# Performance work log

Measured on AMD Instinct MI355X. Metric: run time of the kernel, lower is better.

## Reference

```python
import jax, jax.numpy as jnp
import numpy as np

N = 100000      # num_nodes
E = 6400000     # num edges
D = 128         # embedding_dim
R = 8           # num_roles
ALPHA = 0.15
ITERS = 10

def setup_inputs() -> dict:
    key = jax.random.key(0)
    k1, k2, k3, k4, k5 = jax.random.split(key, 5)
    edge_index = jax.random.randint(k1, (2, E), 0, N)
    batch_nodes = jax.random.randint(k2, (N,), 0, N)
    importance_emb = jax.random.normal(k3, (N, D), dtype=jnp.float32)
    resizer_W = jax.random.normal(k4, (D, 2), dtype=jnp.float32) * (1.0 / np.sqrt(D))
    resizer_b = jnp.zeros((2,), dtype=jnp.float32)
    # xavier_uniform for behavior_matrix [R, 4]
    limit = np.sqrt(6.0 / (R + 4))
    behavior_matrix = jax.random.uniform(k5, (R, 4), minval=-limit, maxval=limit, dtype=jnp.float32)
    return {
        'edge_index': edge_index,
        'batch_nodes': batch_nodes,
        'importance_emb': importance_emb,
        'resizer_W': resizer_W,
        'resizer_b': resizer_b,
        'behavior_matrix': behavior_matrix,
    }

def reference(edge_index, batch_nodes, importance_emb, resizer_W, resizer_b, behavior_matrix):
    src, dst = edge_index[0], edge_index[1]
    num_edges = src.shape[0]
    # out-degrees via segment_sum (== bincount)
    out_deg = jax.ops.segment_sum(jnp.ones((num_edges,), jnp.float32), src, num_segments=N)
    inv_deg_src = 1.0 / jnp.maximum(out_deg, 1.0)[src]  # [E], clamp(min=1)

    # approximate_pagerank: 10 iterations of gather -> scale -> scatter_add
    def body(pr, _):
        contrib = (1.0 - ALPHA) * pr[src] * inv_deg_src
        new_pr = jax.ops.segment_sum(contrib, dst, num_segments=N) + ALPHA / N
        return new_pr, None
    pr0 = jnp.full((N,), 1.0 / N, dtype=jnp.float32)
    pagerank, _ = jax.lax.scan(body, pr0, None, length=ITERS)

    # resizer: single Linear(D, 2)
    emb2 = importance_emb @ resizer_W + resizer_b  # [B, 2]

    # X = [deg[batch], pagerank[batch], emb2] -> [B, 4]
    X = jnp.concatenate([out_deg[batch_nodes][:, None],
                         pagerank[batch_nodes][:, None],
                         emb2], axis=1)

    # lstsq(H.T, X.T): A = H.T is [4, R], underdetermined -> minimum-norm
    # solution Z = A^T (A A^T)^{-1} X^T ; W = Z^T  -> [B, R]
    A = behavior_matrix.T                      # [4, R]
    G = A @ A.T                                # [4, 4]
    W = (A.T @ jnp.linalg.solve(G, X.T)).T     # [B, R]

    # F.normalize(W, p=2, dim=1)
    norm = jnp.linalg.norm(W, axis=1, keepdims=True)
    roles = W / jnp.maximum(norm, 1e-12)
    return roles
```

## Files before the change

### kernel.cpp

```cpp
#include <hip/hip_runtime.h>
#include <math.h>

#define N_NODES 100000
#define N_EDGES 6400000
#define DIM     128
#define NROLES  8
#define ALPHA   0.15f
#define PR_ITERS 10

#define DSH      8
#define DBS      256
#define NDB      391
#define SSH      9
#define SBS      512
#define NSB      196
#define NBT      587
#define NBLK_BIN 512
#define CHUNK    12500
#define SEG      4
#define SBIN     1568
#define CAPS     17408

__global__ void k_prep_M(const float* __restrict__ H, float* __restrict__ Mout) {
    if (threadIdx.x != 0 || blockIdx.x != 0) return;
    double G[4][4];
    for (int i = 0; i < 4; ++i)
        for (int j = 0; j < 4; ++j) {
            double s = 0.0;
            for (int r = 0; r < NROLES; ++r)
                s += (double)H[r * 4 + i] * (double)H[r * 4 + j];
            G[i][j] = s;
        }
    double aug[4][8];
    for (int i = 0; i < 4; ++i)
        for (int j = 0; j < 4; ++j) {
            aug[i][j] = G[i][j];
            aug[i][j + 4] = (i == j) ? 1.0 : 0.0;
        }
    for (int c = 0; c < 4; ++c) {
        int p = c; double best = fabs(aug[c][c]);
        for (int r = c + 1; r < 4; ++r) {
            double v = fabs(aug[r][c]);
            if (v > best) { best = v; p = r; }
        }
        if (p != c)
            for (int j = 0; j < 8; ++j) {
                double t = aug[c][j]; aug[c][j] = aug[p][j]; aug[p][j] = t;
            }
        double piv = aug[c][c];
        for (int j = 0; j < 8; ++j) aug[c][j] /= piv;
        for (int r = 0; r < 4; ++r) {
            if (r == c) continue;
            double f = aug[r][c];
            for (int j = 0; j < 8; ++j) aug[r][j] -= f * aug[c][j];
        }
    }
    for (int r = 0; r < NROLES; ++r)
        for (int k = 0; k < 4; ++k) {
            double s = 0.0;
            for (int j = 0; j < 4; ++j)
                s += (double)H[r * 4 + j] * aug[j][k + 4];
            Mout[r * 4 + k] = (float)s;
        }
}

__global__ __launch_bounds__(256)
void k_hist(const int* __restrict__ src, const int* __restrict__ dst,
            unsigned* __restrict__ counts) {
    __shared__ unsigned h[NBT];
    for (int i = threadIdx.x; i < NBT; i += 256) h[i] = 0;
    __syncthreads();
    int beg = blockIdx.x * CHUNK;
    int t = threadIdx.x;
    int mainEnd = beg + 12288;
    for (int e = beg + t * 4; e < mainEnd; e += 1024) {
        int4 s4 = *(const int4*)(src + e);
        int4 d4 = *(const int4*)(dst + e);
        atomicAdd(&h[((unsigned)d4.x) >> DSH], 1u);
        atomicAdd(&h[((unsigned)d4.y) >> DSH], 1u);
        atomicAdd(&h[((unsigned)d4.z) >> DSH], 1u);
        atomicAdd(&h[((unsigned)d4.w) >> DSH], 1u);
        atomicAdd(&h[NDB + (((unsigned)s4.x) >> SSH)], 1u);
        atomicAdd(&h[NDB + (((unsigned)s4.y) >> SSH)], 1u);
        atomicAdd(&h[NDB + (((unsigned)s4.z) >> SSH)], 1u);
        atomicAdd(&h[NDB + (((unsigned)s4.w) >> SSH)], 1u);
    }
    for (int e = mainEnd + t; e < beg + CHUNK; e += 256) {
        atomicAdd(&h[((unsigned)dst[e]) >> DSH], 1u);
        atomicAdd(&h[NDB + (((unsigned)src[e]) >> SSH)], 1u);
    }
    __syncthreads();
    for (int i = threadIdx.x; i < NBT; i += 256)
        counts[blockIdx.x * NBT + i] = h[i];
}

__global__ __launch_bounds__(512)
void k_scanA(const unsigned* __restrict__ counts, unsigned* __restrict__ offs,
             unsigned* __restrict__ btot) {
    int bucket = blockIdx.x, t = threadIdx.x, lane = t & 63, wv = t >> 6;
    unsigned v = counts[t * NBT + bucket], x = v;
    #pragma unroll
    for (int o = 1; o < 64; o <<= 1) {
        unsigned y = __shfl_up(x, o);
        if (lane >= o) x += y;
    }
    __shared__ unsigned wsum[8];
    if (lane == 63) wsum[wv] = x;
    __syncthreads();
    unsigned carry = 0;
    for (int w = 0; w < wv; ++w) carry += wsum[w];
    x += carry;
    offs[t * NBT + bucket] = x - v;
    if (t == 511) btot[bucket] = x;
}

__global__ __launch_bounds__(512)
void k_scanB(const unsigned* __restrict__ btot, unsigned* __restrict__ bases) {
    int half = blockIdx.x;
    int len  = half ? NSB : NDB;
    int t = threadIdx.x, lane = t & 63, wv = t >> 6;
    unsigned v = (t < len) ? btot[(half ? NDB : 0) + t] : 0u, x = v;
    #pragma unroll
    for (int o = 1; o < 64; o <<= 1) {
        unsigned y = __shfl_up(x, o);
        if (lane >= o) x += y;
    }
    __shared__ unsigned wsum[8];
    if (lane == 63) wsum[wv] = x;
    __syncthreads();
    unsigned carry = 0;
    for (int w = 0; w < wv; ++w) carry += wsum[w];
    x += carry;
    if (t <= len) bases[half * 512 + t] = x - v;
}

__global__ __launch_bounds__(512)
void k_place(const int* __restrict__ src, const int* __restrict__ dst,
             const unsigned* __restrict__ counts, const unsigned* __restrict__ offs,
             const unsigned* __restrict__ bases,
             unsigned* __restrict__ rec, unsigned short* __restrict__ recs) {
    __shared__ unsigned buf[CHUNK];
    __shared__ unsigned loc[NDB + 1];
    __shared__ unsigned cur[NDB];
    __shared__ unsigned wsum[8];
    int t = threadIdx.x, lane = t & 63, wv = t >> 6;
    int blk = blockIdx.x;
    int beg = blk * CHUNK;
    int mainEnd = beg + 12288;

    {
        unsigned c = (t < NDB) ? counts[blk * NBT + t] : 0u;
        unsigned x = c;
        #pragma unroll
        for (int o = 1; o < 64; o <<= 1) {
            unsigned y = __shfl_up(x, o);
            if (lane >= o) x += y;
        }
        if (lane == 63) wsum[wv] = x;
        __syncthreads();
        unsigned carry = 0;
        for (int w = 0; w < wv; ++w) carry += wsum[w];
        x += carry;
        if (t < NDB) { loc[t] = x - c; cur[t] = x - c; }
        if (t == NDB - 1) loc[NDB] = x;
    }
    __syncthreads();
    for (int e = beg + t * 4; e < mainEnd; e += 2048) {
        int4 s4 = *(const int4*)(src + e);
        int4 d4 = *(const int4*)(dst + e);
        #pragma unroll
        for (int k = 0; k < 4; ++k) {
            unsigned s = (unsigned)((&s4.x)[k]);
            unsigned d = (unsigned)((&d4.x)[k]);
            unsigned p = atomicAdd(&cur[d >> DSH], 1u);
            buf[p] = ((d & (DBS - 1)) << 17) | s;
        }
    }
    for (int e = mainEnd + t; e < beg + CHUNK; e += 512) {
        unsigned s = (unsigned)src[e];
        unsigned d = (unsigned)dst[e];
        unsigned p = atomicAdd(&cur[d >> DSH], 1u);
        buf[p] = ((d & (DBS - 1)) << 17) | s;
    }
    __syncthreads();
    for (int i = wv; i < NDB; i += 8) {
        unsigned lo = loc[i], n = loc[i + 1] - lo;
        unsigned gbase = bases[i] + offs[blk * NBT + i];
        for (unsigned j = lane; j < n; j += 64)
            rec[gbase + j] = buf[lo + j];
    }
    __syncthreads();

    {
        unsigned c = (t < NSB) ? counts[blk * NBT + NDB + t] : 0u;
        unsigned x = c;
        #pragma unroll
        for (int o = 1; o < 64; o <<= 1) {
            unsigned y = __shfl_up(x, o);
            if (lane >= o) x += y;
        }
        if (lane == 63) wsum[wv] = x;
        __syncthreads();
        unsigned carry = 0;
        for (int w = 0; w < wv; ++w) carry += wsum[w];
        x += carry;
        if (t < NSB) { loc[t] = x - c; cur[t] = x - c; }
        if (t == NSB - 1) loc[NSB] = x;
    }
    __syncthreads();
    unsigned short* b16 = (unsigned short*)buf;
    for (int e = beg + t * 4; e < mainEnd; e += 2048) {
        int4 s4 = *(const int4*)(src + e);
        #pragma unroll
        for (int k = 0; k < 4; ++k) {
            unsigned s = (unsigned)((&s4.x)[k]);
            unsigned p = atomicAdd(&cur[s >> SSH], 1u);
            b16[p] = (unsigned short)(s & (SBS - 1));
        }
    }
    for (int e = mainEnd + t; e < beg + CHUNK; e += 512) {
        unsigned s = (unsigned)src[e];
        unsigned p = atomicAdd(&cur[s >> SSH], 1u);
        b16[p] = (unsigned short)(s & (SBS - 1));
    }
    __syncthreads();
    for (int i = wv; i < NSB; i += 8) {
        unsigned lo = loc[i], n = loc[i + 1] - lo;
        unsigned gbase = bases[512 + i] + offs[blk * NBT + NDB + i];
        for (unsigned j = lane; j < n; j += 64)
            recs[gbase + j] = b16[lo + j];
    }
}

__global__ __launch_bounds__(256)
void k_count_init(const unsigned short* __restrict__ recs,
                  const unsigned* __restrict__ bases,
                  float* __restrict__ deg, float* __restrict__ s,
                  float* __restrict__ val0) {
    __shared__ unsigned cnt[SBS];
    int t = threadIdx.x;
    cnt[t] = 0; cnt[t + 256] = 0;
    __syncthreads();
    int b = blockIdx.x;
    unsigned st = bases[512 + b], en = bases[512 + b + 1];
    unsigned a = (st + 7u) & ~7u;
    if (a > en) a = en;
    for (unsigned i = st + t; i < a; i += 256)
        atomicAdd(&cnt[recs[i]], 1u);
    unsigned mainN = (en - a) & ~2047u;
    const uint4* rp = (const uint4*)(recs + a);
    for (unsigned i = t; i * 8u < mainN; i += 256) {
        uint4 r = rp[i];
        atomicAdd(&cnt[r.x & 0xFFFFu], 1u); atomicAdd(&cnt[r.x >> 16], 1u);
        atomicAdd(&cnt[r.y & 0xFFFFu], 1u); atomicAdd(&cnt[r.y >> 16], 1u);
        atomicAdd(&cnt[r.z & 0xFFFFu], 1u); atomicAdd(&cnt[r.z >> 16], 1u);
        atomicAdd(&cnt[r.w & 0xFFFFu], 1u); atomicAdd(&cnt[r.w >> 16], 1u);
    }
    for (unsigned i = a + mainN + t; i < en; i += 256)
        atomicAdd(&cnt[recs[i]], 1u);
    __syncthreads();
    #pragma unroll
    for (int k = 0; k < 2; ++k) {
        int v = b * SBS + t + k * 256;
        if (v < N_NODES) {
            float d = (float)cnt[t + k * 256];
            float sv = (1.0f - ALPHA) / fmaxf(d, 1.0f);
            deg[v] = d;
            s[v] = sv;
            val0[v] = sv * (1.0f / (float)N_NODES);
        }
    }
}

__global__ __launch_bounds__(256)
void k_sortL(const unsigned* __restrict__ rec, const unsigned* __restrict__ bases,
             unsigned* __restrict__ rec2) {
    __shared__ unsigned hist[SBIN];
    __shared__ unsigned wsum[4];
    __shared__ unsigned buf[CAPS];
    int t = threadIdx.x, lane = t & 63, wv = t >> 6;
    int b = blockIdx.x;
    unsigned st = bases[b], en = bases[b + 1], n = en - st;
    if (n > CAPS) {
        for (unsigned i = st + t; i < en; i += 256) rec2[i] = rec[i];
        return;
    }
    for (int i = t; i < SBIN; i += 256) hist[i] = 0;
    __syncthreads();
    for (unsigned i = st + t; i < en; i += 256)
        atomicAdd(&hist[(rec[i] & 0x1FFFFu) >> 6], 1u);
    __syncthreads();
    unsigned loc[7], sum = 0;
    #pragma unroll
    for (int k = 0; k < 7; ++k) {
        int idx = t * 7 + k;
        loc[k] = (idx < SBIN) ? hist[idx] : 0u;
        sum += loc[k];
    }
    unsigned x = sum;
    #pragma unroll
    for (int o = 1; o < 64; o <<= 1) {
        unsigned y = __shfl_up(x, o);
        if (lane >= o) x += y;
    }
    if (lane == 63) wsum[wv] = x;
    __syncthreads();
    unsigned carry = 0;
    for (int w = 0; w < wv; ++w) carry += wsum[w];
    unsigned base = carry + x - sum;
    __syncthreads();
    #pragma unroll
    for (int k = 0; k < 7; ++k) {
        int idx = t * 7 + k;
        if (idx < SBIN) hist[idx] = base;
        base += loc[k];
    }
    __syncthreads();
    for (unsigned i = st + t; i < en; i += 256) {
        unsigned r = rec[i];
        unsigned p = atomicAdd(&hist[(r & 0x1FFFFu) >> 6], 1u);
        buf[p] = r;
    }
    __syncthreads();
    for (unsigned i = t; i < n; i += 256) rec2[st + i] = buf[i];
}

__global__ __launch_bounds__(256)
void k_iterS(const unsigned* __restrict__ rec2, const unsigned* __restrict__ bases,
             const float* __restrict__ val, float* __restrict__ partial) {
    __shared__ float acc[DBS];
    int t = threadIdx.x;
    int b = blockIdx.x >> 2, seg = blockIdx.x & 3;
    acc[t] = 0.0f;
    __syncthreads();
    unsigned st = bases[b], en = bases[b + 1], n = en - st;
    unsigned s0 = st + (unsigned)(((unsigned long long)n * (unsigned)seg) >> 2);
    unsigned s1 = st + (unsigned)(((unsigned long long)n * (unsigned)(seg + 1)) >> 2);
    unsigned base = s0;
    for (; base + 2048 <= s1; base += 2048) {
        unsigned r0 = rec2[base + t];
        unsigned r1 = rec2[base + t + 256];
        unsigned r2 = rec2[base + t + 512];
        unsigned r3 = rec2[base + t + 768];
        unsigned r4 = rec2[base + t + 1024];
        unsigned r5 = rec2[base + t + 1280];
        unsigned r6 = rec2[base + t + 1536];
        unsigned r7 = rec2[base + t + 1792];
        float v0 = val[r0 & 0x1FFFFu];
        float v1 = val[r1 & 0x1FFFFu];
        float v2 = val[r2 & 0x1FFFFu];
        float v3 = val[r3 & 0x1FFFFu];
        float v4 = val[r4 & 0x1FFFFu];
        float v5 = val[r5 & 0x1FFFFu];
        float v6 = val[r6 & 0x1FFFFu];
        float v7 = val[r7 & 0x1FFFFu];
        atomicAdd(&acc[r0 >> 17], v0);
        atomicAdd(&acc[r1 >> 17], v1);
        atomicAdd(&acc[r2 >> 17], v2);
        atomicAdd(&acc[r3 >> 17], v3);
        atomicAdd(&acc[r4 >> 17], v4);
        atomicAdd(&acc[r5 >> 17], v5);
        atomicAdd(&acc[r6 >> 17], v6);
        atomicAdd(&acc[r7 >> 17], v7);
    }
    for (unsigned i = base + t; i < s1; i += 256) {
        unsigned r = rec2[i];
        atomicAdd(&acc[r >> 17], val[r & 0x1FFFFu]);
    }
    __syncthreads();
    partial[((unsigned)blockIdx.x << 8) + t] = acc[t];
}

__global__ __launch_bounds__(256)
void k_reduceS(const float* __restrict__ partial, const float* __restrict__ s,
               float* __restrict__ pr, float* __restrict__ valn) {
    int v = blockIdx.x * 256 + threadIdx.x;
    if (v >= N_NODES) return;
    unsigned b = (unsigned)v >> DSH;
    int local = v & (DBS - 1);
    const float* p = partial + ((b * SEG) << 8) + local;
    float sum = p[0] + p[256] + p[512] + p[768];
    float pv = sum + ALPHA / (float)N_NODES;
    pr[v] = pv;
    valn[v] = pv * s[v];
}

__global__ __launch_bounds__(256)
void k_final(const float* __restrict__ emb, const float* __restrict__ rW,
             const float* __restrict__ rb, const int* __restrict__ batch,
             const float* __restrict__ deg, const float* __restrict__ pr,
             const float* __restrict__ M, float* __restrict__ out) {
    int wid  = (blockIdx.x * blockDim.x + threadIdx.x) >> 6;
    int lane = threadIdx.x & 63;
    if (wid >= N_NODES) return;

    const float* row = emb + (size_t)wid * DIM;
    float e0 = row[lane];
    float e1 = row[lane + 64];
    float2 w0 = ((const float2*)rW)[lane];
    float2 w1 = ((const float2*)rW)[lane + 64];
    float a0 = e0 * w0.x + e1 * w1.x;
    float a1 = e0 * w0.y + e1 * w1.y;
    #pragma unroll
    for (int off = 32; off; off >>= 1) {
        a0 += __shfl_xor(a0, off);
        a1 += __shfl_xor(a1, off);
    }

    int bn = batch[wid];
    float x0 = deg[bn];
    float x1 = pr[bn];
    float x2 = a0 + rb[0];
    float x3 = a1 + rb[1];

    float wr = 0.0f;
    if (lane < NROLES) {
        const float* m = M + lane * 4;
        wr = m[0] * x0 + m[1] * x1 + m[2] * x2 + m[3] * x3;
    }
    float sq = wr * wr;
    #pragma unroll
    for (int off = 4; off; off >>= 1) sq += __shfl_xor(sq, off);
    float inv = 1.0f / fmaxf(sqrtf(sq), 1e-12f);
    if (lane < NROLES) out[(size_t)wid * NROLES + lane] = wr * inv;
}

extern "C" void kernel_launch(void* const* d_in, const int* in_sizes, int n_in,
                              void* d_out, int out_size, void* d_ws, size_t ws_size,
                              hipStream_t stream) {
    const int*   edge  = (const int*)d_in[0];
    const int*   src   = edge;
    const int*   dst   = edge + N_EDGES;
    const int*   batch = (const int*)d_in[1];
    const float* emb   = (const float*)d_in[2];
    const float* rW    = (const float*)d_in[3];
    const float* rb    = (const float*)d_in[4];
    const float* H     = (const float*)d_in[5];
    float*       out   = (float*)d_out;

    float*    deg    = (float*)d_ws;
    float*    s      = deg   + 100352;
    float*    pr     = s     + 100352;
    float*    valA   = pr    + 100352;
    float*    valB   = valA  + 100352;
    float*    M      = valB  + 100352;
    unsigned* counts = (unsigned*)(M + 32);
    unsigned* offs   = counts + NBLK_BIN * NBT;
    unsigned* btot   = offs   + NBLK_BIN * NBT;
    unsigned* bases  = btot   + 1024;
    unsigned* rec    = bases  + 1024;
    unsigned* rec2   = rec    + N_EDGES;
    unsigned short* recs = (unsigned short*)rec2;
    float*    partial = (float*)(rec2 + N_EDGES);

    k_prep_M<<<1, 1, 0, stream>>>(H, M);

    k_hist <<<NBLK_BIN, 256, 0, stream>>>(src, dst, counts);
    k_scanA<<<NBT,      512, 0, stream>>>(counts, offs, btot);
    k_scanB<<<2,        512, 0, stream>>>(btot, bases);
    k_place<<<NBLK_BIN, 512, 0, stream>>>(src, dst, counts, offs, bases, rec, recs);
    k_count_init<<<NSB, 256, 0, stream>>>(recs, bases, deg, s, valA);
    k_sortL<<<NDB,      256, 0, stream>>>(rec, bases, rec2);

    float* vcur = valA;
    float* vnxt = valB;
    for (int it = 0; it < PR_ITERS; ++it) {
        k_iterS <<<NDB * SEG, 256, 0, stream>>>(rec2, bases, vcur, partial);
        k_reduceS<<<NDB, 256, 0, stream>>>(partial, s, pr, vnxt);
        float* t = vcur; vcur = vnxt; vnxt = t;
    }

    const int FG = (N_NODES + 3) / 4;
    k_final<<<FG, 256, 0, stream>>>(emb, rW, rb, batch, deg, pr, M, out);
}
```

Baseline: 555.6 us.

## Sort edges by destination within bucket and reduce runs with wave segmented scan

The local sort inside each destination bucket now keys on the destination slot instead of on source ranges, so edges that share a destination become contiguous. The PageRank iteration kernel then combines each run of equal destinations with a wavefront segmented scan and issues one shared-memory atomic per run. This replaces the per-edge LDS atomics. The trade-off is that gathers of val become scattered rather than source-local, which may hurt cache locality, and the scan adds shuffle work per edge. The matrix-prep kernel is also folded into the scanB launch as an extra block, removing one launch.

```diff
diff --git a/kernel.cpp b/kernel.cpp
--- a/kernel.cpp
+++ b/kernel.cpp
@@ -18,51 +18,7 @@
 #define NBLK_BIN 512
 #define CHUNK    12500
 #define SEG      4
-#define SBIN     1568
 #define CAPS     17408
-
-__global__ void k_prep_M(const float* __restrict__ H, float* __restrict__ Mout) {
-    if (threadIdx.x != 0 || blockIdx.x != 0) return;
-    double G[4][4];
-    for (int i = 0; i < 4; ++i)
-        for (int j = 0; j < 4; ++j) {
-            double s = 0.0;
-            for (int r = 0; r < NROLES; ++r)
-                s += (double)H[r * 4 + i] * (double)H[r * 4 + j];
-            G[i][j] = s;
-        }
-    double aug[4][8];
-    for (int i = 0; i < 4; ++i)
-        for (int j = 0; j < 4; ++j) {
-            aug[i][j] = G[i][j];
-            aug[i][j + 4] = (i == j) ? 1.0 : 0.0;
-        }
-    for (int c = 0; c < 4; ++c) {
-        int p = c; double best = fabs(aug[c][c]);
-        for (int r = c + 1; r < 4; ++r) {
-            double v = fabs(aug[r][c]);
-            if (v > best) { best = v; p = r; }
-        }
-        if (p != c)
-            for (int j = 0; j < 8; ++j) {
-                double t = aug[c][j]; aug[c][j] = aug[p][j]; aug[p][j] = t;
-            }
-        double piv = aug[c][c];
-        for (int j = 0; j < 8; ++j) aug[c][j] /= piv;
-        for (int r = 0; r < 4; ++r) {
-            if (r == c) continue;
-            double f = aug[r][c];
-            for (int j = 0; j < 8; ++j) aug[r][j] -= f * aug[c][j];
-        }
-    }
-    for (int r = 0; r < NROLES; ++r)
-        for (int k = 0; k < 4; ++k) {
-            double s = 0.0;
-            for (int j = 0; j < 4; ++j)
-                s += (double)H[r * 4 + j] * aug[j][k + 4];
-            Mout[r * 4 + k] = (float)s;
-        }
-}
 
 __global__ __launch_bounds__(256)
 void k_hist(const int* __restrict__ src, const int* __restrict__ dst,
@@ -115,7 +71,51 @@
 }
 
 __global__ __launch_bounds__(512)
-void k_scanB(const unsigned* __restrict__ btot, unsigned* __restrict__ bases) {
+void k_scanB(const unsigned* __restrict__ btot, unsigned* __restrict__ bases,
+             const float* __restrict__ H, float* __restrict__ Mout) {
+    if (blockIdx.x == 2) {
+        if (threadIdx.x != 0) return;
+        double G[4][4];
+        for (int i = 0; i < 4; ++i)
+            for (int j = 0; j < 4; ++j) {
+                double s = 0.0;
+                for (int r = 0; r < NROLES; ++r)
+                    s += (double)H[r * 4 + i] * (double)H[r * 4 + j];
+                G[i][j] = s;
+            }
+        double aug[4][8];
+        for (int i = 0; i < 4; ++i)
+            for (int j = 0; j < 4; ++j) {
+                aug[i][j] = G[i][j];
+                aug[i][j + 4] = (i == j) ? 1.0 : 0.0;
+            }
+        for (int c = 0; c < 4; ++c) {
+            int p = c; double best = fabs(aug[c][c]);
+            for (int r = c + 1; r < 4; ++r) {
+                double v = fabs(aug[r][c]);
+                if (v > best) { best = v; p = r; }
+            }
+            if (p != c)
+                for (int j = 0; j < 8; ++j) {
+                    double tt = aug[c][j]; aug[c][j] = aug[p][j]; aug[p][j] = tt;
+                }
+            double piv = aug[c][c];
+            for (int j = 0; j < 8; ++j) aug[c][j] /= piv;
+            for (int r = 0; r < 4; ++r) {
+                if (r == c) continue;
+                double f = aug[r][c];
+                for (int j = 0; j < 8; ++j) aug[r][j] -= f * aug[c][j];
+            }
+        }
+        for (int r = 0; r < NROLES; ++r)
+            for (int k = 0; k < 4; ++k) {
+                double s = 0.0;
+                for (int j = 0; j < 4; ++j)
+                    s += (double)H[r * 4 + j] * aug[j][k + 4];
+                Mout[r * 4 + k] = (float)s;
+            }
+        return;
+    }
     int half = blockIdx.x;
     int len  = half ? NSB : NDB;
     int t = threadIdx.x, lane = t & 63, wv = t >> 6;
@@ -273,9 +273,9 @@
 }
 
 __global__ __launch_bounds__(256)
-void k_sortL(const unsigned* __restrict__ rec, const unsigned* __restrict__ bases,
+void k_sortD(const unsigned* __restrict__ rec, const unsigned* __restrict__ bases,
              unsigned* __restrict__ rec2) {
-    __shared__ unsigned hist[SBIN];
+    __shared__ unsigned hist[DBS];
     __shared__ unsigned wsum[4];
     __shared__ unsigned buf[CAPS];
     int t = threadIdx.x, lane = t & 63, wv = t >> 6;
@@ -285,19 +285,12 @@
         for (unsigned i = st + t; i < en; i += 256) rec2[i] = rec[i];
         return;
     }
-    for (int i = t; i < SBIN; i += 256) hist[i] = 0;
+    hist[t] = 0;
     __syncthreads();
     for (unsigned i = st + t; i < en; i += 256)
-        atomicAdd(&hist[(rec[i] & 0x1FFFFu) >> 6], 1u);
-    __syncthreads();
-    unsigned loc[7], sum = 0;
-    #pragma unroll
-    for (int k = 0; k < 7; ++k) {
-        int idx = t * 7 + k;
-        loc[k] = (idx < SBIN) ? hist[idx] : 0u;
-        sum += loc[k];
-    }
-    unsigned x = sum;
+        atomicAdd(&hist[rec[i] >> 17], 1u);
+    __syncthreads();
+    unsigned c = hist[t], x = c;
     #pragma unroll
     for (int o = 1; o < 64; o <<= 1) {
         unsigned y = __shfl_up(x, o);
@@ -307,18 +300,12 @@
     __syncthreads();
     unsigned carry = 0;
     for (int w = 0; w < wv; ++w) carry += wsum[w];
-    unsigned base = carry + x - sum;
-    __syncthreads();
-    #pragma unroll
-    for (int k = 0; k < 7; ++k) {
-        int idx = t * 7 + k;
-        if (idx < SBIN) hist[idx] = base;
-        base += loc[k];
-    }
+    x += carry;
+    hist[t] = x - c;
     __syncthreads();
     for (unsigned i = st + t; i < en; i += 256) {
         unsigned r = rec[i];
-        unsigned p = atomicAdd(&hist[(r & 0x1FFFFu) >> 6], 1u);
+        unsigned p = atomicAdd(&hist[r >> 17], 1u);
         buf[p] = r;
     }
     __syncthreads();
@@ -326,46 +313,37 @@
 }
 
 __global__ __launch_bounds__(256)
-void k_iterS(const unsigned* __restrict__ rec2, const unsigned* __restrict__ bases,
+void k_iterD(const unsigned* __restrict__ rec2, const unsigned* __restrict__ bases,
              const float* __restrict__ val, float* __restrict__ partial) {
     __shared__ float acc[DBS];
-    int t = threadIdx.x;
+    int t = threadIdx.x, lane = t & 63;
     int b = blockIdx.x >> 2, seg = blockIdx.x & 3;
     acc[t] = 0.0f;
     __syncthreads();
     unsigned st = bases[b], en = bases[b + 1], n = en - st;
     unsigned s0 = st + (unsigned)(((unsigned long long)n * (unsigned)seg) >> 2);
     unsigned s1 = st + (unsigned)(((unsigned long long)n * (unsigned)(seg + 1)) >> 2);
-    unsigned base = s0;
-    for (; base + 2048 <= s1; base += 2048) {
-        unsigned r0 = rec2[base + t];
-        unsigned r1 = rec2[base + t + 256];
-        unsigned r2 = rec2[base + t + 512];
-        unsigned r3 = rec2[base + t + 768];
-        unsigned r4 = rec2[base + t + 1024];
-        unsigned r5 = rec2[base + t + 1280];
-        unsigned r6 = rec2[base + t + 1536];
-        unsigned r7 = rec2[base + t + 1792];
-        float v0 = val[r0 & 0x1FFFFu];
-        float v1 = val[r1 & 0x1FFFFu];
-        float v2 = val[r2 & 0x1FFFFu];
-        float v3 = val[r3 & 0x1FFFFu];
-        float v4 = val[r4 & 0x1FFFFu];
-        float v5 = val[r5 & 0x1FFFFu];
-        float v6 = val[r6 & 0x1FFFFu];
-        float v7 = val[r7 & 0x1FFFFu];
-        atomicAdd(&acc[r0 >> 17], v0);
-        atomicAdd(&acc[r1 >> 17], v1);
-        atomicAdd(&acc[r2 >> 17], v2);
-        atomicAdd(&acc[r3 >> 17], v3);
-        atomicAdd(&acc[r4 >> 17], v4);
-        atomicAdd(&acc[r5 >> 17], v5);
-        atomicAdd(&acc[r6 >> 17], v6);
-        atomicAdd(&acc[r7 >> 17], v7);
-    }
-    for (unsigned i = base + t; i < s1; i += 256) {
-        unsigned r = rec2[i];
-        atomicAdd(&acc[r >> 17], val[r & 0x1FFFFu]);
+    for (unsigned base = s0; base < s1; base += 256) {
+        unsigned i = base + t;
+        bool ok = (i < s1);
+        unsigned r = ok ? rec2[i] : 0xFFFFFFFFu;
+        float v = ok ? val[r & 0x1FFFFu] : 0.0f;
+        unsigned k = r >> 17;
+        unsigned kp = __shfl_up(k, 1);
+        bool head = (lane == 0) || (kp != k);
+        unsigned long long hmask = __ballot(head);
+        float x = v;
+        #pragma unroll
+        for (int off = 1; off < 64; off <<= 1) {
+            float y = __shfl_up(x, off);
+            if (lane >= off) x += y;
+        }
+        unsigned long long le = (~0ull) >> (63 - lane);
+        int H = 63 - __clzll(hmask & le);
+        float prev = __shfl(x, H - 1);
+        float runsum = x - ((H == 0) ? 0.0f : prev);
+        bool tail = (lane == 63) || (((hmask >> lane) >> 1) & 1ull);
+        if (tail && ok) atomicAdd(&acc[k], runsum);
     }
     __syncthreads();
     partial[((unsigned)blockIdx.x << 8) + t] = acc[t];
@@ -453,19 +431,17 @@
     unsigned short* recs = (unsigned short*)rec2;
     float*    partial = (float*)(rec2 + N_EDGES);
 
-    k_prep_M<<<1, 1, 0, stream>>>(H, M);
-
     k_hist <<<NBLK_BIN, 256, 0, stream>>>(src, dst, counts);
     k_scanA<<<NBT,      512, 0, stream>>>(counts, offs, btot);
-    k_scanB<<<2,        512, 0, stream>>>(btot, bases);
+    k_scanB<<<3,        512, 0, stream>>>(btot, bases, H, M);
     k_place<<<NBLK_BIN, 512, 0, stream>>>(src, dst, counts, offs, bases, rec, recs);
     k_count_init<<<NSB, 256, 0, stream>>>(recs, bases, deg, s, valA);
-    k_sortL<<<NDB,      256, 0, stream>>>(rec, bases, rec2);
+    k_sortD<<<NDB,      256, 0, stream>>>(rec, bases, rec2);
 
     float* vcur = valA;
     float* vnxt = valB;
     for (int it = 0; it < PR_ITERS; ++it) {
-        k_iterS <<<NDB * SEG, 256, 0, stream>>>(rec2, bases, vcur, partial);
+        k_iterD <<<NDB * SEG, 256, 0, stream>>>(rec2, bases, vcur, partial);
         k_reduceS<<<NDB, 256, 0, stream>>>(partial, s, pr, vnxt);
         float* t = vcur; vcur = vnxt; vnxt = t;
     }
```

Result: faster. 463.5 us (median of 2 runs) (-16.6%).
